# Performance work log

Hardware: AMD Instinct MI355X
Metric: run time of the kernel (lower is better)

The kernel has to match this reference:

```python
import jax, jax.numpy as jnp
import numpy as np

H = 64  # hidden_size
IN = 1  # input_size
OUT = 32  # fc output


def _lstm_layer(x, Wih, Whh, bih, bhh):
    """x: (B,T,D_in). Returns (outputs (B,T,H), final h (B,H)). PyTorch gate order i,f,g,o."""
    B = x.shape[0]
    b = bih + bhh  # (4H,)
    # precompute input contributions for all timesteps: (T,B,4H)
    xW = jnp.einsum('btd,gd->tbg', x, Wih) + b

    def step(carry, xw_t):
        h, c = carry
        gates = xw_t + h @ Whh.T  # (B,4H)
        i, f, g, o = jnp.split(gates, 4, axis=-1)
        i = jax.nn.sigmoid(i)
        f = jax.nn.sigmoid(f)
        g = jnp.tanh(g)
        o = jax.nn.sigmoid(o)
        c = f * c + i * g
        h = o * jnp.tanh(c)
        return (h, c), h

    h0 = jnp.zeros((B, H), dtype=x.dtype)
    c0 = jnp.zeros((B, H), dtype=x.dtype)
    (h_T, _), hs = jax.lax.scan(step, (h0, c0), xW)
    return jnp.swapaxes(hs, 0, 1), h_T


def setup_inputs() -> dict:
    key = jax.random.key(0)
    ks = jax.random.split(key, 11)
    s_ih0 = 1.0 / np.sqrt(H)
    inp = {
        'x': jax.random.normal(ks[0], (2048, 512, IN), dtype=jnp.float32),
        # layer 0: input_size -> H
        'Wih0': jax.random.uniform(ks[1], (4 * H, IN), minval=-s_ih0, maxval=s_ih0),
        'Whh0': jax.random.uniform(ks[2], (4 * H, H), minval=-s_ih0, maxval=s_ih0),
        'bih0': jax.random.uniform(ks[3], (4 * H,), minval=-s_ih0, maxval=s_ih0),
        'bhh0': jax.random.uniform(ks[4], (4 * H,), minval=-s_ih0, maxval=s_ih0),
        # layer 1: H -> H
        'Wih1': jax.random.uniform(ks[5], (4 * H, H), minval=-s_ih0, maxval=s_ih0),
        'Whh1': jax.random.uniform(ks[6], (4 * H, H), minval=-s_ih0, maxval=s_ih0),
        'bih1': jax.random.uniform(ks[7], (4 * H,), minval=-s_ih0, maxval=s_ih0),
        'bhh1': jax.random.uniform(ks[8], (4 * H,), minval=-s_ih0, maxval=s_ih0),
        # fc: H -> 32
        'fcW': jax.random.uniform(ks[9], (OUT, H), minval=-s_ih0, maxval=s_ih0),
        'fcb': jax.random.uniform(ks[10], (OUT,), minval=-s_ih0, maxval=s_ih0),
    }
    return inp


def reference(x, Wih0, Whh0, bih0, bhh0, Wih1, Whh1, bih1, bhh1, fcW, fcb):
    h1_seq, _ = _lstm_layer(x, Wih0, Whh0, bih0, bhh0)
    _, h_last = _lstm_layer(h1_seq, Wih1, Whh1, bih1, bhh1)  # hidden[-1]
    features = jax.nn.relu(h_last @ fcW.T + fcb)  # (B, 32)
    return features
```

## Files before the change

kernel.cpp:

```cpp
#include <hip/hip_runtime.h>
#include <hip/hip_bf16.h>


#define HID 64
#define TSTEPS 512
#define MB 8
#define RS 80

typedef _Float16 f16x8 __attribute__((ext_vector_type(8)));
typedef float f32x4 __attribute__((ext_vector_type(4)));
typedef float f32x2 __attribute__((ext_vector_type(2)));

#define KSIG (-1.44269504089f)
#define KTANH (2.88539008178f)

__device__ __forceinline__ f32x2 mk2(float a, float b) { f32x2 r; r[0] = a; r[1] = b; return r; }
__device__ __forceinline__ f32x2 exp2v(f32x2 v) {
    f32x2 r; r[0] = __builtin_amdgcn_exp2f(v[0]); r[1] = __builtin_amdgcn_exp2f(v[1]); return r;
}
__device__ __forceinline__ f32x2 rcpv(f32x2 v) {
    f32x2 r; r[0] = __builtin_amdgcn_rcpf(v[0]); r[1] = __builtin_amdgcn_rcpf(v[1]); return r;
}

__global__ __launch_bounds__(512, 1) void lstm_feat_kernel(
    const float* __restrict__ x,
    const float* __restrict__ Wih0, const float* __restrict__ Whh0,
    const float* __restrict__ bih0, const float* __restrict__ bhh0,
    const float* __restrict__ Wih1, const float* __restrict__ Whh1,
    const float* __restrict__ bih1, const float* __restrict__ bhh1,
    const float* __restrict__ fcW, const float* __restrict__ fcb,
    float* __restrict__ out)
{
    __shared__ float x_lds[(MB / 2) * TSTEPS * 2];
    __shared__ __align__(16) _Float16 h0_lds[2][MB * RS];
    __shared__ __align__(16) _Float16 h1_lds[2][MB * RS];
    __shared__ float h1f32[MB * HID];
    __shared__ float fcw_lds[HID * 32];
    __shared__ float fcb_lds[32];

    const int tid  = threadIdx.x;
    const int wave = tid >> 6;
    const int lane = tid & 63;
    const int nq   = lane & 15;
    const int quad = lane >> 4;
    const int bbase = blockIdx.x * MB;
    const bool isL1 = (wave >= 4);
    const int ug = wave & 3;
    const int u  = ug * 16 + nq;

    for (int i = tid; i < TSTEPS * MB; i += 512) {
        int r = i >> 9, t = i & (TSTEPS - 1);
        x_lds[(r >> 1) * (TSTEPS * 2) + t * 2 + (r & 1)] = x[(bbase + r) * TSTEPS + t];
    }
    for (int i = tid; i < 32 * HID; i += 512) {
        int o = i >> 6, kk = i & 63;
        fcw_lds[kk * 32 + o] = fcW[i];
    }
    if (tid < 32) fcb_lds[tid] = fcb[tid];
    for (int i = tid; i < 2 * MB * RS; i += 512) {
        ((_Float16*)h0_lds)[i] = (_Float16)0.f;
        ((_Float16*)h1_lds)[i] = (_Float16)0.f;
    }

    f16x8 wA[4][2], wB[4][2];
    f32x4 cbias[4];
    float wx0s[4];
    {
        const float* Wa = isL1 ? Wih1 : Whh0;
        const float* Wb = isL1 ? Whh1 : Whh0;
        const float* bi = isL1 ? bih1 : bih0;
        const float* bh = isL1 ? bhh1 : bhh0;
        #pragma unroll
        for (int g = 0; g < 4; ++g) {
            const float sc = (g == 2) ? KTANH : KSIG;
            const int n = g * 64 + u;
            const float bs = (bi[n] + bh[n]) * sc;
            cbias[g] = (f32x4){bs, bs, bs, bs};
            wx0s[g] = Wih0[n] * sc;
            #pragma unroll
            for (int ks = 0; ks < 2; ++ks) {
                const int k0 = quad * 8 + ks * 32;
                f16x8 a, b;
                #pragma unroll
                for (int j = 0; j < 8; ++j) {
                    a[j] = (_Float16)(Wa[n * HID + k0 + j] * sc);
                    b[j] = (_Float16)(Wb[n * HID + k0 + j] * sc);
                }
                wA[g][ks] = a; wB[g][ks] = b;
            }
        }
    }

    const f32x4 zero4 = {0.f, 0.f, 0.f, 0.f};
    const int arow = (nq >> 1) * RS + quad * 8;
    const int b0r  = (quad * 2) * RS;
    const int hbase = quad * 2;
    f32x2 cc = mk2(0.f, 0.f);

    __syncthreads();

#define FCELL(PI, PF, PG, PO, HH) do {                                               \
    f32x2 ea = exp2v(PI), eb = exp2v(PF), eg = exp2v(PG), ed = exp2v(PO);            \
    f32x2 Aq = ea + 1.f, Bq = eb + 1.f, Gp = eg + 1.f, Dn = ed + 1.f;                \
    f32x2 AG = Aq * Gp;                                                              \
    f32x2 r1 = rcpv(AG * Bq);                                                        \
    f32x2 nm = cc * AG + (eg - 1.f) * Bq;                                            \
    cc = nm * r1;                                                                    \
    f32x2 E  = exp2v(cc * KTANH);                                                    \
    f32x2 r2 = rcpv(Dn * (E + 1.f));                                                 \
    HH = (E - 1.f) * r2;                                                             \
} while (0)

#define L0_SUB(P, Q, XQ2) do {                                                       \
    f16x8 a0_ = *(const f16x8*)&h0_lds[P][arow];                                     \
    f16x8 a1_ = *(const f16x8*)&h0_lds[P][arow + 32];                                \
    f32x4 ac[4];                                                                     \
    __builtin_amdgcn_s_setprio(1);                                                   \
    _Pragma("unroll")                                                                \
    for (int g = 0; g < 4; ++g)                                                      \
        ac[g] = __builtin_amdgcn_mfma_f32_16x16x32_f16(a0_, wA[g][0], cbias[g], 0, 0, 0); \
    _Pragma("unroll")                                                                \
    for (int g = 0; g < 4; ++g)                                                      \
        ac[g] = __builtin_amdgcn_mfma_f32_16x16x32_f16(a1_, wA[g][1], ac[g], 0, 0, 0); \
    __builtin_amdgcn_s_setprio(0);                                                   \
    f32x2 pi = (XQ2) * wx0s[0] + mk2(ac[0][0], ac[0][2]);                            \
    f32x2 pf = (XQ2) * wx0s[1] + mk2(ac[1][0], ac[1][2]);                            \
    f32x2 pg = (XQ2) * wx0s[2] + mk2(ac[2][0], ac[2][2]);                            \
    f32x2 po = (XQ2) * wx0s[3] + mk2(ac[3][0], ac[3][2]);                            \
    f32x2 hh;                                                                        \
    FCELL(pi, pf, pg, po, hh);                                                       \
    h0_lds[Q][b0r + u]      = (_Float16)hh[0];                                       \
    h0_lds[Q][b0r + RS + u] = (_Float16)hh[1];                                       \
} while (0)

#define L1_SUB(P, Q, GUARD) do {                                                     \
    f16x8 a00 = *(const f16x8*)&h0_lds[P][arow];                                     \
    f16x8 a01 = *(const f16x8*)&h0_lds[P][arow + 32];                                \
    f16x8 a10 = *(const f16x8*)&h1_lds[P][arow];                                     \
    f16x8 a11 = *(const f16x8*)&h1_lds[P][arow + 32];                                \
    f32x4 aA[4], aB[4];                                                              \
    __builtin_amdgcn_s_setprio(1);                                                   \
    _Pragma("unroll")                                                                \
    for (int g = 0; g < 4; ++g)                                                      \
        aA[g] = __builtin_amdgcn_mfma_f32_16x16x32_f16(a00, wA[g][0], zero4, 0, 0, 0); \
    _Pragma("unroll")                                                                \
    for (int g = 0; g < 4; ++g)                                                      \
        aB[g] = __builtin_amdgcn_mfma_f32_16x16x32_f16(a10, wB[g][0], cbias[g], 0, 0, 0); \
    _Pragma("unroll")                                                                \
    for (int g = 0; g < 4; ++g)                                                      \
        aA[g] = __builtin_amdgcn_mfma_f32_16x16x32_f16(a01, wA[g][1], aA[g], 0, 0, 0); \
    _Pragma("unroll")                                                                \
    for (int g = 0; g < 4; ++g)                                                      \
        aB[g] = __builtin_amdgcn_mfma_f32_16x16x32_f16(a11, wB[g][1], aB[g], 0, 0, 0); \
    __builtin_amdgcn_s_setprio(0);                                                   \
    if (GUARD) {                                                                     \
        f32x2 pi = mk2(aA[0][0], aA[0][2]) + mk2(aB[0][0], aB[0][2]);                \
        f32x2 pf = mk2(aA[1][0], aA[1][2]) + mk2(aB[1][0], aB[1][2]);                \
        f32x2 pg = mk2(aA[2][0], aA[2][2]) + mk2(aB[2][0], aB[2][2]);                \
        f32x2 po = mk2(aA[3][0], aA[3][2]) + mk2(aB[3][0], aB[3][2]);                \
        f32x2 hh;                                                                    \
        FCELL(pi, pf, pg, po, hh);                                                   \
        h1_lds[Q][b0r + u]      = (_Float16)hh[0];                                   \
        h1_lds[Q][b0r + RS + u] = (_Float16)hh[1];                                   \
    }                                                                                \
} while (0)

    const int xoff = quad * (TSTEPS * 2);
    for (int k = 0; k < TSTEPS; k += 2) {
        f32x2 xa, xb;
        if (!isL1) {
            const f32x4 xv = *(const f32x4*)&x_lds[xoff + k * 2];
            xa = mk2(xv[0], xv[1]); xb = mk2(xv[2], xv[3]);
            L0_SUB(0, 1, xa);
        } else {
            L1_SUB(0, 1, (k > 0));
        }
        __syncthreads();
        if (!isL1) {
            L0_SUB(1, 0, xb);
        } else {
            L1_SUB(1, 0, true);
        }
        __syncthreads();
    }

    if (isL1) {
        f16x8 a00 = *(const f16x8*)&h0_lds[0][arow];
        f16x8 a01 = *(const f16x8*)&h0_lds[0][arow + 32];
        f16x8 a10 = *(const f16x8*)&h1_lds[0][arow];
        f16x8 a11 = *(const f16x8*)&h1_lds[0][arow + 32];
        f32x4 aA[4], aB[4];
        #pragma unroll
        for (int g = 0; g < 4; ++g)
            aA[g] = __builtin_amdgcn_mfma_f32_16x16x32_f16(a00, wA[g][0], zero4, 0, 0, 0);
        #pragma unroll
        for (int g = 0; g < 4; ++g)
            aB[g] = __builtin_amdgcn_mfma_f32_16x16x32_f16(a10, wB[g][0], cbias[g], 0, 0, 0);
        #pragma unroll
        for (int g = 0; g < 4; ++g)
            aA[g] = __builtin_amdgcn_mfma_f32_16x16x32_f16(a01, wA[g][1], aA[g], 0, 0, 0);
        #pragma unroll
        for (int g = 0; g < 4; ++g)
            aB[g] = __builtin_amdgcn_mfma_f32_16x16x32_f16(a11, wB[g][1], aB[g], 0, 0, 0);
        f32x2 pi = mk2(aA[0][0], aA[0][2]) + mk2(aB[0][0], aB[0][2]);
        f32x2 pf = mk2(aA[1][0], aA[1][2]) + mk2(aB[1][0], aB[1][2]);
        f32x2 pg = mk2(aA[2][0], aA[2][2]) + mk2(aB[2][0], aB[2][2]);
        f32x2 po = mk2(aA[3][0], aA[3][2]) + mk2(aB[3][0], aB[3][2]);
        f32x2 hh;
        FCELL(pi, pf, pg, po, hh);
        h1f32[hbase * HID + u]       = hh[0];
        h1f32[(hbase + 1) * HID + u] = hh[1];
    }
    __syncthreads();

    if (tid < MB * 32) {
        const int o  = tid & 31;
        const int rr = tid >> 5;
        float acc = fcb_lds[o];
        #pragma unroll 8
        for (int kk = 0; kk < HID; ++kk)
            acc += h1f32[rr * HID + kk] * fcw_lds[kk * 32 + o];
        out[(bbase + rr) * 32 + o] = fmaxf(acc, 0.f);
    }
}

extern "C" void kernel_launch(void* const* d_in, const int* in_sizes, int n_in,
                              void* d_out, int out_size, void* d_ws, size_t ws_size,
                              hipStream_t stream) {
    const float* x    = (const float*)d_in[0];
    const float* Wih0 = (const float*)d_in[1];
    const float* Whh0 = (const float*)d_in[2];
    const float* bih0 = (const float*)d_in[3];
    const float* bhh0 = (const float*)d_in[4];
    const float* Wih1 = (const float*)d_in[5];
    const float* Whh1 = (const float*)d_in[6];
    const float* bih1 = (const float*)d_in[7];
    const float* bhh1 = (const float*)d_in[8];
    const float* fcW  = (const float*)d_in[9];
    const float* fcb  = (const float*)d_in[10];
    float* out = (float*)d_out;

    lstm_feat_kernel<<<2048 / MB, 512, 0, stream>>>(
        x, Wih0, Whh0, bih0, bhh0, Wih1, Whh1, bih1, bhh1, fcW, fcb, out);
}
```

Before: 303.3 us.

## Halve batch per block, use 4-wave blocks with two blocks per CU

Cuts the per-block batch from 8 to 4 and the block size from 512 to 256 threads, with each wave now computing 32 hidden units across all four gates and using 8 MFMA tiles. The input-x contribution is folded into the MFMA accumulator init instead of being added afterwards. Layer roles are swapped by block parity, and launch bounds allow two blocks per CU so that the latency of independent recurrences can overlap. The cost is that each wave issues twice as many MFMAs per step, holds more weight registers, and wastes more MFMA rows because only 4 batch rows fill a 16-row tile.

New measurement: 401.4 us. 1.32x slower.

```diff
diff --git a/kernel.cpp b/kernel.cpp
--- a/kernel.cpp
+++ b/kernel.cpp
@@ -4,7 +4,7 @@
 
 #define HID 64
 #define TSTEPS 512
-#define MB 8
+#define MB 4
 #define RS 80
 
 typedef _Float16 f16x8 __attribute__((ext_vector_type(8)));
@@ -22,7 +22,9 @@
     f32x2 r; r[0] = __builtin_amdgcn_rcpf(v[0]); r[1] = __builtin_amdgcn_rcpf(v[1]); return r;
 }
 
-__global__ __launch_bounds__(512, 1) void lstm_feat_kernel(
+#define MFMA16(A, B, C) __builtin_amdgcn_mfma_f32_16x16x32_f16((A), (B), (C), 0, 0, 0)
+
+__global__ __launch_bounds__(256, 2) void lstm_feat_kernel(
     const float* __restrict__ x,
     const float* __restrict__ Wih0, const float* __restrict__ Whh0,
     const float* __restrict__ bih0, const float* __restrict__ bhh0,
@@ -31,7 +33,7 @@
     const float* __restrict__ fcW, const float* __restrict__ fcb,
     float* __restrict__ out)
 {
-    __shared__ float x_lds[(MB / 2) * TSTEPS * 2];
+    __shared__ __align__(16) float x_lds[MB * TSTEPS];
     __shared__ __align__(16) _Float16 h0_lds[2][MB * RS];
     __shared__ __align__(16) _Float16 h1_lds[2][MB * RS];
     __shared__ float h1f32[MB * HID];
@@ -44,58 +46,69 @@
     const int nq   = lane & 15;
     const int quad = lane >> 4;
     const int bbase = blockIdx.x * MB;
-    const bool isL1 = (wave >= 4);
-    const int ug = wave & 3;
-    const int u  = ug * 16 + nq;
-
-    for (int i = tid; i < TSTEPS * MB; i += 512) {
+    const bool isL1 = ((wave >> 1) ^ (blockIdx.x & 1)) != 0;
+    const int U0 = (wave & 1) * 32;
+
+    for (int i = tid; i < MB * TSTEPS; i += 256) {
         int r = i >> 9, t = i & (TSTEPS - 1);
-        x_lds[(r >> 1) * (TSTEPS * 2) + t * 2 + (r & 1)] = x[(bbase + r) * TSTEPS + t];
-    }
-    for (int i = tid; i < 32 * HID; i += 512) {
+        x_lds[r * TSTEPS + t] = x[(bbase + r) * TSTEPS + t];
+    }
+    for (int i = tid; i < 32 * HID; i += 256) {
         int o = i >> 6, kk = i & 63;
         fcw_lds[kk * 32 + o] = fcW[i];
     }
     if (tid < 32) fcb_lds[tid] = fcb[tid];
-    for (int i = tid; i < 2 * MB * RS; i += 512) {
+    for (int i = tid; i < 2 * MB * RS; i += 256) {
         ((_Float16*)h0_lds)[i] = (_Float16)0.f;
         ((_Float16*)h1_lds)[i] = (_Float16)0.f;
     }
 
-    f16x8 wA[4][2], wB[4][2];
-    f32x4 cbias[4];
-    float wx0s[4];
+    f16x8 wA[8][2], wB[8][2];
+    float bs0[8], wx0[8];
     {
         const float* Wa = isL1 ? Wih1 : Whh0;
-        const float* Wb = isL1 ? Whh1 : Whh0;
         const float* bi = isL1 ? bih1 : bih0;
         const float* bh = isL1 ? bhh1 : bhh0;
         #pragma unroll
-        for (int g = 0; g < 4; ++g) {
+        for (int t = 0; t < 8; ++t) {
+            const int g = t & 3, hh = t >> 2;
+            const int n = g * 64 + U0 + hh * 16 + nq;
             const float sc = (g == 2) ? KTANH : KSIG;
-            const int n = g * 64 + u;
-            const float bs = (bi[n] + bh[n]) * sc;
-            cbias[g] = (f32x4){bs, bs, bs, bs};
-            wx0s[g] = Wih0[n] * sc;
+            bs0[t] = (bi[n] + bh[n]) * sc;
+            wx0[t] = Wih0[n] * sc;
             #pragma unroll
             for (int ks = 0; ks < 2; ++ks) {
                 const int k0 = quad * 8 + ks * 32;
-                f16x8 a, b;
+                f16x8 a;
                 #pragma unroll
-                for (int j = 0; j < 8; ++j) {
+                for (int j = 0; j < 8; ++j)
                     a[j] = (_Float16)(Wa[n * HID + k0 + j] * sc);
-                    b[j] = (_Float16)(Wb[n * HID + k0 + j] * sc);
-                }
-                wA[g][ks] = a; wB[g][ks] = b;
+                wA[t][ks] = a;
             }
         }
-    }
-
-    const f32x4 zero4 = {0.f, 0.f, 0.f, 0.f};
-    const int arow = (nq >> 1) * RS + quad * 8;
-    const int b0r  = (quad * 2) * RS;
-    const int hbase = quad * 2;
-    f32x2 cc = mk2(0.f, 0.f);
+        if (isL1) {
+            #pragma unroll
+            for (int t = 0; t < 8; ++t) {
+                const int g = t & 3, hh = t >> 2;
+                const int n = g * 64 + U0 + hh * 16 + nq;
+                const float sc = (g == 2) ? KTANH : KSIG;
+                #pragma unroll
+                for (int ks = 0; ks < 2; ++ks) {
+                    const int k0 = quad * 8 + ks * 32;
+                    f16x8 b;
+                    #pragma unroll
+                    for (int j = 0; j < 8; ++j)
+                        b[j] = (_Float16)(Whh1[n * HID + k0 + j] * sc);
+                    wB[t][ks] = b;
+                }
+            }
+        }
+    }
+
+    const int arow = (nq >> 2) * RS + quad * 8;
+    const int wad  = quad * RS + U0 + nq;
+    float cc0 = 0.f, cc1 = 0.f;
+    f32x2 cc = mk2(cc0, cc1);
 
     __syncthreads();
 
@@ -111,26 +124,28 @@
     HH = (E - 1.f) * r2;                                                             \
 } while (0)
 
-#define L0_SUB(P, Q, XQ2) do {                                                       \
-    f16x8 a0_ = *(const f16x8*)&h0_lds[P][arow];                                     \
-    f16x8 a1_ = *(const f16x8*)&h0_lds[P][arow + 32];                                \
-    f32x4 ac[4];                                                                     \
+#define L0_SUB(P, Q, XS) do {                                                        \
+    f16x8 a0 = *(const f16x8*)&h0_lds[P][arow];                                      \
+    f16x8 a1 = *(const f16x8*)&h0_lds[P][arow + 32];                                 \
+    f32x4 ac[8];                                                                     \
     __builtin_amdgcn_s_setprio(1);                                                   \
     _Pragma("unroll")                                                                \
-    for (int g = 0; g < 4; ++g)                                                      \
-        ac[g] = __builtin_amdgcn_mfma_f32_16x16x32_f16(a0_, wA[g][0], cbias[g], 0, 0, 0); \
-    _Pragma("unroll")                                                                \
-    for (int g = 0; g < 4; ++g)                                                      \
-        ac[g] = __builtin_amdgcn_mfma_f32_16x16x32_f16(a1_, wA[g][1], ac[g], 0, 0, 0); \
+    for (int t = 0; t < 8; ++t) {                                                    \
+        const float cv = fmaf((XS), wx0[t], bs0[t]);                                 \
+        f32x4 C = {cv, cv, cv, cv};                                                  \
+        ac[t] = MFMA16(a0, wA[t][0], C);                                             \
+    }                                                                                \
+    _Pragma("unroll")                                                                \
+    for (int t = 0; t < 8; ++t) ac[t] = MFMA16(a1, wA[t][1], ac[t]);                 \
     __builtin_amdgcn_s_setprio(0);                                                   \
-    f32x2 pi = (XQ2) * wx0s[0] + mk2(ac[0][0], ac[0][2]);                            \
-    f32x2 pf = (XQ2) * wx0s[1] + mk2(ac[1][0], ac[1][2]);                            \
-    f32x2 pg = (XQ2) * wx0s[2] + mk2(ac[2][0], ac[2][2]);                            \
-    f32x2 po = (XQ2) * wx0s[3] + mk2(ac[3][0], ac[3][2]);                            \
+    f32x2 pi = mk2(ac[0][0], ac[4][0]);                                              \
+    f32x2 pf = mk2(ac[1][0], ac[5][0]);                                              \
+    f32x2 pg = mk2(ac[2][0], ac[6][0]);                                              \
+    f32x2 po = mk2(ac[3][0], ac[7][0]);                                              \
     f32x2 hh;                                                                        \
     FCELL(pi, pf, pg, po, hh);                                                       \
-    h0_lds[Q][b0r + u]      = (_Float16)hh[0];                                       \
-    h0_lds[Q][b0r + RS + u] = (_Float16)hh[1];                                       \
+    h0_lds[Q][wad]      = (_Float16)hh[0];                                           \
+    h0_lds[Q][wad + 16] = (_Float16)hh[1];                                           \
 } while (0)
 
 #define L1_SUB(P, Q, GUARD) do {                                                     \
@@ -138,49 +153,39 @@
     f16x8 a01 = *(const f16x8*)&h0_lds[P][arow + 32];                                \
     f16x8 a10 = *(const f16x8*)&h1_lds[P][arow];                                     \
     f16x8 a11 = *(const f16x8*)&h1_lds[P][arow + 32];                                \
-    f32x4 aA[4], aB[4];                                                              \
+    f32x4 ac[8];                                                                     \
     __builtin_amdgcn_s_setprio(1);                                                   \
     _Pragma("unroll")                                                                \
-    for (int g = 0; g < 4; ++g)                                                      \
-        aA[g] = __builtin_amdgcn_mfma_f32_16x16x32_f16(a00, wA[g][0], zero4, 0, 0, 0); \
-    _Pragma("unroll")                                                                \
-    for (int g = 0; g < 4; ++g)                                                      \
-        aB[g] = __builtin_amdgcn_mfma_f32_16x16x32_f16(a10, wB[g][0], cbias[g], 0, 0, 0); \
-    _Pragma("unroll")                                                                \
-    for (int g = 0; g < 4; ++g)                                                      \
-        aA[g] = __builtin_amdgcn_mfma_f32_16x16x32_f16(a01, wA[g][1], aA[g], 0, 0, 0); \
-    _Pragma("unroll")                                                                \
-    for (int g = 0; g < 4; ++g)                                                      \
-        aB[g] = __builtin_amdgcn_mfma_f32_16x16x32_f16(a11, wB[g][1], aB[g], 0, 0, 0); \
+    for (int t = 0; t < 8; ++t) {                                                    \
+        f32x4 C = {bs0[t], bs0[t], bs0[t], bs0[t]};                                  \
+        ac[t] = MFMA16(a00, wA[t][0], C);                                            \
+    }                                                                                \
+    _Pragma("unroll")                                                                \
+    for (int t = 0; t < 8; ++t) ac[t] = MFMA16(a01, wA[t][1], ac[t]);                \
+    _Pragma("unroll")                                                                \
+    for (int t = 0; t < 8; ++t) ac[t] = MFMA16(a10, wB[t][0], ac[t]);                \
+    _Pragma("unroll")                                                                \
+    for (int t = 0; t < 8; ++t) ac[t] = MFMA16(a11, wB[t][1], ac[t]);                \
     __builtin_amdgcn_s_setprio(0);                                                   \
     if (GUARD) {                                                                     \
-        f32x2 pi = mk2(aA[0][0], aA[0][2]) + mk2(aB[0][0], aB[0][2]);                \
-        f32x2 pf = mk2(aA[1][0], aA[1][2]) + mk2(aB[1][0], aB[1][2]);                \
-        f32x2 pg = mk2(aA[2][0], aA[2][2]) + mk2(aB[2][0], aB[2][2]);                \
-        f32x2 po = mk2(aA[3][0], aA[3][2]) + mk2(aB[3][0], aB[3][2]);                \
+        f32x2 pi = mk2(ac[0][0], ac[4][0]);                                          \
+        f32x2 pf = mk2(ac[1][0], ac[5][0]);                                          \
+        f32x2 pg = mk2(ac[2][0], ac[6][0]);                                          \
+        f32x2 po = mk2(ac[3][0], ac[7][0]);                                          \
         f32x2 hh;                                                                    \
         FCELL(pi, pf, pg, po, hh);                                                   \
-        h1_lds[Q][b0r + u]      = (_Float16)hh[0];                                   \
-        h1_lds[Q][b0r + RS + u] = (_Float16)hh[1];                                   \
+        h1_lds[Q][wad]      = (_Float16)hh[0];                                       \
+        h1_lds[Q][wad + 16] = (_Float16)hh[1];                                       \
     }                                                                                \
 } while (0)
 
-    const int xoff = quad * (TSTEPS * 2);
+    const int xoff = quad * TSTEPS;
     for (int k = 0; k < TSTEPS; k += 2) {
-        f32x2 xa, xb;
-        if (!isL1) {
-            const f32x4 xv = *(const f32x4*)&x_lds[xoff + k * 2];
-            xa = mk2(xv[0], xv[1]); xb = mk2(xv[2], xv[3]);
-            L0_SUB(0, 1, xa);
-        } else {
-            L1_SUB(0, 1, (k > 0));
-        }
+        f32x2 xv;
+        if (!isL1) xv = *(const f32x2*)&x_lds[xoff + k];
+        if (!isL1) { L0_SUB(0, 1, xv[0]); } else { L1_SUB(0, 1, (k > 0)); }
         __syncthreads();
-        if (!isL1) {
-            L0_SUB(1, 0, xb);
-        } else {
-            L1_SUB(1, 0, true);
-        }
+        if (!isL1) { L0_SUB(1, 0, xv[1]); } else { L1_SUB(1, 0, true); }
         __syncthreads();
     }
 
@@ -189,27 +194,26 @@
         f16x8 a01 = *(const f16x8*)&h0_lds[0][arow + 32];
         f16x8 a10 = *(const f16x8*)&h1_lds[0][arow];
         f16x8 a11 = *(const f16x8*)&h1_lds[0][arow + 32];
-        f32x4 aA[4], aB[4];
-        #pragma unroll
-        for (int g = 0; g < 4; ++g)
-            aA[g] = __builtin_amdgcn_mfma_f32_16x16x32_f16(a00, wA[g][0], zero4, 0, 0, 0);
-        #pragma unroll
-        for (int g = 0; g < 4; ++g)
-            aB[g] = __builtin_amdgcn_mfma_f32_16x16x32_f16(a10, wB[g][0], cbias[g], 0, 0, 0);
-        #pragma unroll
-        for (int g = 0; g < 4; ++g)
-            aA[g] = __builtin_amdgcn_mfma_f32_16x16x32_f16(a01, wA[g][1], aA[g], 0, 0, 0);
-        #pragma unroll
-        for (int g = 0; g < 4; ++g)
-            aB[g] = __builtin_amdgcn_mfma_f32_16x16x32_f16(a11, wB[g][1], aB[g], 0, 0, 0);
-        f32x2 pi = mk2(aA[0][0], aA[0][2]) + mk2(aB[0][0], aB[0][2]);
-        f32x2 pf = mk2(aA[1][0], aA[1][2]) + mk2(aB[1][0], aB[1][2]);
-        f32x2 pg = mk2(aA[2][0], aA[2][2]) + mk2(aB[2][0], aB[2][2]);
-        f32x2 po = mk2(aA[3][0], aA[3][2]) + mk2(aB[3][0], aB[3][2]);
+        f32x4 ac[8];
+        #pragma unroll
+        for (int t = 0; t < 8; ++t) {
+            f32x4 C = {bs0[t], bs0[t], bs0[t], bs0[t]};
+            ac[t] = MFMA16(a00, wA[t][0], C);
+        }
+        #pragma unroll
+        for (int t = 0; t < 8; ++t) ac[t] = MFMA16(a01, wA[t][1], ac[t]);
+        #pragma unroll
+        for (int t = 0; t < 8; ++t) ac[t] = MFMA16(a10, wB[t][0], ac[t]);
+        #pragma unroll
+        for (int t = 0; t < 8; ++t) ac[t] = MFMA16(a11, wB[t][1], ac[t]);
+        f32x2 pi = mk2(ac[0][0], ac[4][0]);
+        f32x2 pf = mk2(ac[1][0], ac[5][0]);
+        f32x2 pg = mk2(ac[2][0], ac[6][0]);
+        f32x2 po = mk2(ac[3][0], ac[7][0]);
         f32x2 hh;
         FCELL(pi, pf, pg, po, hh);
-        h1f32[hbase * HID + u]       = hh[0];
-        h1f32[(hbase + 1) * HID + u] = hh[1];
+        h1f32[quad * HID + U0 + nq]      = hh[0];
+        h1f32[quad * HID + U0 + 16 + nq] = hh[1];
     }
     __syncthreads();
 
@@ -240,6 +244,6 @@
     const float* fcb  = (const float*)d_in[10];
     float* out = (float*)d_out;
 
-    lstm_feat_kernel<<<2048 / MB, 512, 0, stream>>>(
+    lstm_feat_kernel<<<2048 / MB, 256, 0, stream>>>(
         x, Wih0, Whh0, bih0, bhh0, Wih1, Whh1, bih1, bhh1, fcW, fcb, out);
 }
```
